# Performance work log

Measured on AMD Instinct MI355X. Metric: run time of the kernel, lower is better.

## Reference

```python
import jax, jax.numpy as jnp
import numpy as np

D_MODEL = 1024
N_HEADS = 16
D_HEAD = D_MODEL // N_HEADS
BLOCK = 128
B, T = 2, 2048


def setup_inputs() -> dict:
    key = jax.random.key(0)
    ks = jax.random.split(key, 5)
    x = jax.random.normal(ks[0], (B, T, D_MODEL), dtype=jnp.float32)
    def init_w(k):
        # nn.Linear default init scale ~ 1/sqrt(fan_in)
        return jax.random.normal(k, (D_MODEL, D_MODEL), dtype=jnp.float32) / np.sqrt(D_MODEL).astype(np.float32)
    return {
        "x": x,
        "Wq": init_w(ks[1]),
        "Wk": init_w(ks[2]),
        "Wv": init_w(ks[3]),
        "Wo": init_w(ks[4]),
    }


def _flash_attention(Q, K, V, block_size, scale):
    """Online-softmax tiled attention over kv blocks (causal). Q,K,V: (B,H,T,d)."""
    Bb, H, Tt, d = Q.shape
    n_blocks = Tt // block_size
    # (n_blocks, B, H, block, d) so scan streams kv tiles
    Kb = K.reshape(Bb, H, n_blocks, block_size, d).transpose(2, 0, 1, 3, 4)
    Vb = V.reshape(Bb, H, n_blocks, block_size, d).transpose(2, 0, 1, 3, 4)
    starts = jnp.arange(n_blocks) * block_size
    q_pos = jnp.arange(Tt)

    def step(carry, xs):
        m, l, acc = carry
        kb, vb, st = xs
        # scores: (B,H,T,block)
        scores = scale * jnp.einsum('bhtd,bhsd->bhts', Q, kb)
        kv_pos = st + jnp.arange(block_size)
        future = kv_pos[None, :] > q_pos[:, None]          # (T, block)
        scores = jnp.where(future[None, None], -jnp.inf, scores)
        m_new = jnp.maximum(m, jnp.max(scores, axis=-1, keepdims=True))
        p = jnp.exp(scores - m_new)
        corr = jnp.exp(m - m_new)
        l = corr * l + jnp.sum(p, axis=-1, keepdims=True)
        acc = corr * acc + jnp.einsum('bhts,bhsd->bhtd', p, vb)
        return (m_new, l, acc), None

    m0 = jnp.full((Bb, H, Tt, 1), -jnp.inf, dtype=jnp.float32)
    l0 = jnp.zeros((Bb, H, Tt, 1), dtype=jnp.float32)
    a0 = jnp.zeros((Bb, H, Tt, d), dtype=jnp.float32)
    (m, l, acc), _ = jax.lax.scan(step, (m0, l0, a0), (Kb, Vb, starts))
    return acc / jnp.maximum(l, 1e-12)


def reference(x, Wq, Wk, Wv, Wo):
    Bx, Tx, _ = x.shape
    scale = 1.0 / np.sqrt(D_HEAD).astype(np.float32)
    def proj(W):  # nn.Linear: y = x @ W.T
        y = jnp.einsum('btm,nm->btn', x, W)
        return y.reshape(Bx, Tx, N_HEADS, D_HEAD).transpose(0, 2, 1, 3)
    Q, K, V = proj(Wq), proj(Wk), proj(Wv)
    O = _flash_attention(Q.astype(jnp.float32), K.astype(jnp.float32), V.astype(jnp.float32), BLOCK, scale)
    O = O.astype(x.dtype).transpose(0, 2, 1, 3).reshape(Bx, Tx, D_MODEL)
    return jnp.einsum('btm,nm->btn', O, Wo)
```

## Files before the change

kernel.cpp:

```cpp
#include <hip/hip_runtime.h>
#include <hip/hip_bf16.h>

typedef __attribute__((ext_vector_type(8))) short short8;
typedef __attribute__((ext_vector_type(4))) float f32x4;
typedef __attribute__((ext_vector_type(16))) float f32x16;
typedef __attribute__((ext_vector_type(2))) unsigned int uint2v;
typedef __attribute__((ext_vector_type(4))) unsigned int uint4v;
typedef unsigned short u16;

#define MFMA_BF16(a, b, c) __builtin_amdgcn_mfma_f32_16x16x32_bf16(a, b, c, 0, 0, 0)
#define MFMA32(a, b, c) __builtin_amdgcn_mfma_f32_32x32x16_bf16(a, b, c, 0, 0, 0)

#define T_SEQ 2048
#define DMODEL 1024
#define NHEADS 16
#define DHEAD 64
#define NEG_BIG (-30000.0f)
#define QSCALE 0.1803368801111f
#define RESCALE_THR 8.0f

#if __has_builtin(__builtin_amdgcn_exp2f)
#define EXP2(x) __builtin_amdgcn_exp2f(x)
#else
#define EXP2(x) exp2f(x)
#endif

__device__ __forceinline__ unsigned bfr(unsigned u) {
  return (u + 0x7fffu + ((u >> 16) & 1u)) >> 16;
}
__device__ __forceinline__ uint4v ld8bf(const float* __restrict__ p) {
  const uint4v a = *(const uint4v*)p;
  const uint4v b = *(const uint4v*)(p + 4);
  uint4v r;
  r[0] = bfr(a[0]) | (bfr(a[1]) << 16);
  r[1] = bfr(a[2]) | (bfr(a[3]) << 16);
  r[2] = bfr(b[0]) | (bfr(b[1]) << 16);
  r[3] = bfr(b[2]) | (bfr(b[3]) << 16);
  return r;
}
__device__ __forceinline__ u16 f2bf(float f) {
  unsigned u = __float_as_uint(f);
  u += 0x7fffu + ((u >> 16) & 1u);
  return (u16)(u >> 16);
}
__device__ __forceinline__ unsigned pk2(float a, float b) {
  return (__float_as_uint(a) >> 16) | (__float_as_uint(b) & 0xffff0000u);
}
__device__ __forceinline__ void gld16(const u16* g, u16* l) {
  __builtin_amdgcn_global_load_lds(
      (const __attribute__((address_space(1))) unsigned int*)g,
      (__attribute__((address_space(3))) unsigned int*)l, 16, 0, 0);
}

__global__ __launch_bounds__(256) void cvt_all(
    const float* __restrict__ x, const float* __restrict__ wq,
    const float* __restrict__ wk, const float* __restrict__ wv,
    const float* __restrict__ wo, u16* __restrict__ xh, u16* __restrict__ wqh,
    u16* __restrict__ wkh, u16* __restrict__ wvh, u16* __restrict__ woh) {
  int bi = blockIdx.x;
  const float* s;
  u16* d;
  size_t base;
  if (bi < 2048) {
    s = x; d = xh; base = (size_t)bi * 2048;
  } else {
    int k = (bi - 2048) >> 9;
    int r = (bi - 2048) & 511;
    s = (k == 0) ? wq : (k == 1) ? wk : (k == 2) ? wv : wo;
    d = (k == 0) ? wqh : (k == 1) ? wkh : (k == 2) ? wvh : woh;
    base = (size_t)r * 2048;
  }
  size_t i = base + (size_t)threadIdx.x * 8;
  *(uint4v*)&d[i] = ld8bf(&s[i]);
}

__global__ __launch_bounds__(256) void gemm_qkv(
    const u16* __restrict__ X, const u16* __restrict__ Wq,
    const u16* __restrict__ Wk, const u16* __restrict__ Wv,
    u16* __restrict__ Qo, u16* __restrict__ Ko, u16* __restrict__ Vo) {
  __shared__ __attribute__((aligned(16))) u16 sm[16384];
  const int tid = threadIdx.x, lane = tid & 63, w = tid >> 6;
  const int wm = (w >> 1) * 64, wn = (w & 1) * 64;
  const int lrow = lane & 15;
  const int lk = (lane >> 4) << 3;
  const int lq = (lane >> 4) << 2;

  const int id = blockIdx.x;
  const int xcd = id & 7, r8 = id >> 3;
  const int xo = r8 & 3, yz = r8 >> 2;
  const int y = yz & 7, z = yz >> 3;
  const int mBase = (xcd * 4 + xo) * 128, nBase = y * 128;

  const u16* Bt = (z == 0) ? Wq : (z == 1) ? Wk : Wv;
  u16* D = (z == 0) ? Qo : (z == 1) ? Ko : Vo;
  const float scale = (z == 0) ? QSCALE : 1.0f;

  f32x4 acc[4][4];
#pragma unroll
  for (int mi = 0; mi < 4; mi++)
#pragma unroll
    for (int ni = 0; ni < 4; ni++) acc[mi][ni] = (f32x4)0.0f;

  auto stage = [&](int buf, int k0) {
#pragma unroll
    for (int i = 0; i < 2; i++) {
      int c = i * 256 + tid;
      int r = c >> 2, kk = (c & 3) << 3;
      gld16(&X[(size_t)(mBase + r) * 1024 + k0 + kk], &sm[buf * 4096 + c * 8]);
      gld16(&Bt[(size_t)(nBase + r) * 1024 + k0 + kk],
            &sm[8192 + buf * 4096 + c * 8]);
    }
  };

  stage(0, 0);
  __syncthreads();
  int cur = 0;
  for (int k0 = 0; k0 < 1024; k0 += 32) {
    if (k0 + 32 < 1024) stage(cur ^ 1, k0 + 32);
    short8 af[4], bf[4];
#pragma unroll
    for (int mi = 0; mi < 4; mi++)
      af[mi] = *(const short8*)&sm[cur * 4096 + (wm + mi * 16 + lrow) * 32 + lk];
#pragma unroll
    for (int ni = 0; ni < 4; ni++)
      bf[ni] =
          *(const short8*)&sm[8192 + cur * 4096 + (wn + ni * 16 + lrow) * 32 + lk];
#pragma unroll
    for (int mi = 0; mi < 4; mi++)
#pragma unroll
      for (int ni = 0; ni < 4; ni++)
        acc[mi][ni] = MFMA_BF16(af[mi], bf[ni], acc[mi][ni]);
    __syncthreads();
    cur ^= 1;
  }

  if (z != 2) {
#pragma unroll
    for (int mi = 0; mi < 4; mi++)
#pragma unroll
      for (int r = 0; r < 4; r++) {
        int m = mBase + wm + mi * 16 + lq + r;
        int b = m >> 11, t = m & 2047;
#pragma unroll
        for (int ni = 0; ni < 4; ni++) {
          int n = nBase + wn + ni * 16 + lrow;
          int h = n >> 6, dd = n & 63;
          D[(((size_t)(b * NHEADS + h)) * T_SEQ + t) * DHEAD + dd] =
              f2bf(acc[mi][ni][r] * scale);
        }
      }
  } else {
    u16* TT = &sm[w * 4096];
#pragma unroll
    for (int mi = 0; mi < 4; mi++)
#pragma unroll
      for (int r = 0; r < 4; r++) {
        int t_loc = mi * 16 + lq + r;
#pragma unroll
        for (int ni = 0; ni < 4; ni++) {
          int d_loc = ni * 16 + lrow;
          TT[d_loc * 64 + ((((t_loc >> 3) ^ (d_loc & 7)) << 3) | (t_loc & 7))] =
              f2bf(acc[mi][ni][r]);
        }
      }
    const int b = (mBase + wm) >> 11;
    const int t0 = (mBase + wm) & 2047;
#pragma unroll
    for (int it = 0; it < 8; it++) {
      int d_loc = it * 8 + (lane >> 3);
      int ch = lane & 7;
      short8 v = *(const short8*)&TT[d_loc * 64 + ((ch ^ (d_loc & 7)) << 3)];
      int n = nBase + wn + d_loc;
      int h = n >> 6, dd = n & 63;
      *(uint4v*)&D[(((size_t)((b * NHEADS + h) * DHEAD + dd)) * T_SEQ) + t0 +
                   ch * 8] = *(const uint4v*)&v;
    }
  }
}

__global__ __launch_bounds__(512, 4) void attn_qt32(
    const u16* __restrict__ Qg, const u16* __restrict__ Kg,
    const u16* __restrict__ Vtg, u16* __restrict__ Ob) {
  __shared__ __attribute__((aligned(16))) u16 smem[32768];

  const int tid = threadIdx.x;
  const int w = tid >> 6, lane = tid & 63;
  const int g = w >> 2;
  const int wg = w & 3;
  const int l31 = lane & 31, h = lane >> 5;
  const int rsw = l31 & 7;

  const int id = blockIdx.x;
  const int half = id >> 8;
  const int x = id & 255;
  const int xcd = x & 7;
  const int u = x >> 3;
  const int bh = xcd * 4 + (u & 3);
  const int qp = u >> 2;
  const int qt = half ? (15 - qp) : qp;
  const int b = bh >> 4, hh = bh & 15;
  const int qb = qt << 7;
  const u16* Qp = Qg + (size_t)bh * T_SEQ * DHEAD;
  const u16* Kp = Kg + (size_t)bh * T_SEQ * DHEAD;
  const u16* Vp = Vtg + (size_t)bh * DHEAD * T_SEQ;
  const int lastT = 2 * qt + 1;

  auto stage_tile = [&](int T) {
    if (T > lastT) return;
    const int slot = T & 3;
    const int r = tid >> 3;
    const int sw = ((tid & 7) ^ (r & 7)) << 3;
    gld16(&Kp[(size_t)(T * 64 + r) * DHEAD + sw], &smem[slot * 4096 + tid * 8]);
    gld16(&Vp[(size_t)r * T_SEQ + T * 64 + sw],
          &smem[16384 + slot * 4096 + tid * 8]);
  };

  stage_tile(0);
  stage_tile(1);

  const int qg = qb + wg * 32 + l31;
  short8 qf[4];
#pragma unroll
  for (int ks = 0; ks < 4; ks++)
    qf[ks] = *(const short8*)&Qp[(size_t)qg * DHEAD + ks * 16 + h * 8];

  float mst = NEG_BIG, lst = 0.f;
  f32x16 oa0 = (f32x16)0.f, oa1 = (f32x16)0.f;
  __syncthreads();

  for (int s = 0; s <= qt; s++) {
    stage_tile(2 * s + 2);
    stage_tile(2 * s + 3);
    const int T = 2 * s + g;
    const u16* Kc = &smem[(T & 3) * 4096];
    const u16* Vc = &smem[16384 + (T & 3) * 4096];

#pragma unroll
    for (int kvt2 = 0; kvt2 < 2; kvt2++) {
      f32x16 S = (f32x16)0.f;
      __builtin_amdgcn_s_setprio(1);
#pragma unroll
      for (int ks = 0; ks < 4; ks++) {
        short8 kf = *(const short8*)&Kc[(kvt2 * 32 + l31) * 64 +
                                        (((ks * 2 + h) ^ rsw) << 3)];
        S = MFMA32(kf, qf[ks], S);
      }
      __builtin_amdgcn_s_setprio(0);

      if (s == qt) {
        const int kvb2 = T * 64 + kvt2 * 32 + 4 * h;
#pragma unroll
        for (int r = 0; r < 16; r++) {
          int kv = kvb2 + (r & 3) + 8 * (r >> 2);
          if (kv > qg) S[r] = NEG_BIG;
        }
      }

      float mx = NEG_BIG;
#pragma unroll
      for (int r = 0; r < 16; r += 4)
        mx = fmaxf(mx, fmaxf(fmaxf(S[r], S[r + 1]), fmaxf(S[r + 2], S[r + 3])));
      mx = fmaxf(mx, __shfl_xor(mx, 32));
      if (!__all(mx <= mst + RESCALE_THR)) {
        float mn = fmaxf(mst, mx);
        float corr = EXP2(mst - mn);
        mst = mn;
        lst *= corr;
#pragma unroll
        for (int r = 0; r < 16; r++) {
          oa0[r] *= corr;
          oa1[r] *= corr;
        }
      }
      float ls = 0.f;
#pragma unroll
      for (int r = 0; r < 16; r++) {
        float pv = EXP2(S[r] - mst);
        S[r] = pv;
        ls += pv;
      }
      ls += __shfl_xor(ls, 32);
      lst += ls;

#pragma unroll
      for (int ks2 = 0; ks2 < 2; ks2++) {
        unsigned P0 = pk2(S[8 * ks2 + 0], S[8 * ks2 + 1]);
        unsigned P1 = pk2(S[8 * ks2 + 2], S[8 * ks2 + 3]);
        unsigned P2 = pk2(S[8 * ks2 + 4], S[8 * ks2 + 5]);
        unsigned P3 = pk2(S[8 * ks2 + 6], S[8 * ks2 + 7]);
        unsigned R0 = __shfl_xor(P0, 32), R1 = __shfl_xor(P1, 32);
        unsigned R2 = __shfl_xor(P2, 32), R3 = __shfl_xor(P3, 32);
        uint4v fu;
        fu[0] = h ? R2 : P0;
        fu[1] = h ? R3 : P1;
        fu[2] = h ? P2 : R0;
        fu[3] = h ? P3 : R1;
        short8 pf = *(short8*)&fu;
        const int kgr = kvt2 * 4 + ks2 * 2 + h;
        __builtin_amdgcn_s_setprio(1);
        short8 vf0 = *(const short8*)&Vc[l31 * 64 + ((kgr ^ rsw) << 3)];
        oa0 = MFMA32(vf0, pf, oa0);
        short8 vf1 = *(const short8*)&Vc[(32 + l31) * 64 + ((kgr ^ rsw) << 3)];
        oa1 = MFMA32(vf1, pf, oa1);
        __builtin_amdgcn_s_setprio(0);
      }
    }
    __syncthreads();
  }

  float* O1 = (float*)smem;
  float* ml = (float*)&smem[16384];
  const int q = wg * 32 + l31;
  if (g == 1) {
#pragma unroll
    for (int dt = 0; dt < 2; dt++)
#pragma unroll
      for (int t4 = 0; t4 < 4; t4++) {
        int gr = dt * 8 + t4 * 2 + h;
        int swg = (gr & 8) | ((gr & 7) ^ (q & 7));
        f32x4 v;
#pragma unroll
        for (int j = 0; j < 4; j++) v[j] = dt ? oa1[t4 * 4 + j] : oa0[t4 * 4 + j];
        *(f32x4*)&O1[q * 64 + swg * 4] = v;
      }
    if (h == 0) {
      ml[q] = mst;
      ml[128 + q] = lst;
    }
  }
  __syncthreads();
  if (g == 0) {
    const float m1 = ml[q], l1 = ml[128 + q];
    const float M = fmaxf(mst, m1);
    const float c0 = EXP2(mst - M), c1 = EXP2(m1 - M);
    const float inv = 1.f / (c0 * lst + c1 * l1);
    size_t rowbase = ((size_t)(b * T_SEQ + qb + q)) * DMODEL + hh * DHEAD;
#pragma unroll
    for (int dt = 0; dt < 2; dt++)
#pragma unroll
      for (int t4 = 0; t4 < 4; t4++) {
        int gr = dt * 8 + t4 * 2 + h;
        int swg = (gr & 8) | ((gr & 7) ^ (q & 7));
        f32x4 o1 = *(const f32x4*)&O1[q * 64 + swg * 4];
        float a0 = (c0 * (dt ? oa1[t4 * 4 + 0] : oa0[t4 * 4 + 0]) + c1 * o1[0]) * inv;
        float a1 = (c0 * (dt ? oa1[t4 * 4 + 1] : oa0[t4 * 4 + 1]) + c1 * o1[1]) * inv;
        float a2 = (c0 * (dt ? oa1[t4 * 4 + 2] : oa0[t4 * 4 + 2]) + c1 * o1[2]) * inv;
        float a3 = (c0 * (dt ? oa1[t4 * 4 + 3] : oa0[t4 * 4 + 3]) + c1 * o1[3]) * inv;
        uint2v pk;
        pk[0] = (unsigned)f2bf(a0) | ((unsigned)f2bf(a1) << 16);
        pk[1] = (unsigned)f2bf(a2) | ((unsigned)f2bf(a3) << 16);
        *(uint2v*)&Ob[rowbase + dt * 32 + t4 * 8 + 4 * h] = pk;
      }
  }
}

__global__ __launch_bounds__(256) void gemm_out_bf(const u16* __restrict__ O,
                                                   const u16* __restrict__ Wo,
                                                   float* __restrict__ Out) {
  __shared__ __attribute__((aligned(16))) u16 As[2][128 * 32];
  __shared__ __attribute__((aligned(16))) u16 Bs[2][64 * 32];
  const int tid = threadIdx.x, lane = tid & 63, w = tid >> 6;
  const int wm = (w >> 1) * 64, wn = (w & 1) * 32;
  const int lrow = lane & 15;
  const int lk = (lane >> 4) << 3;
  const int lq = (lane >> 4) << 2;

  const int id = blockIdx.x;
  const int xcd = id & 7, r8 = id >> 3;
  const int xo = r8 & 3, y = r8 >> 2;
  const int mBase = (xcd * 4 + xo) * 128, nBase = y * 64;

  f32x4 acc[4][2];
#pragma unroll
  for (int mi = 0; mi < 4; mi++)
#pragma unroll
    for (int ni = 0; ni < 2; ni++) acc[mi][ni] = (f32x4)0.0f;

  auto stage = [&](int buf, int k0) {
#pragma unroll
    for (int i = 0; i < 2; i++) {
      int c = i * 256 + tid;
      int r = c >> 2, kk = (c & 3) << 3;
      gld16(&O[(size_t)(mBase + r) * 1024 + k0 + kk], &As[buf][c * 8]);
    }
    int r = tid >> 2, kk = (tid & 3) << 3;
    gld16(&Wo[(size_t)(nBase + r) * 1024 + k0 + kk], &Bs[buf][tid * 8]);
  };

  stage(0, 0);
  __syncthreads();
  int cur = 0;
  for (int k0 = 0; k0 < 1024; k0 += 32) {
    if (k0 + 32 < 1024) stage(cur ^ 1, k0 + 32);
    short8 af[4], bf[2];
#pragma unroll
    for (int mi = 0; mi < 4; mi++)
      af[mi] = *(const short8*)&As[cur][(wm + mi * 16 + lrow) * 32 + lk];
#pragma unroll
    for (int ni = 0; ni < 2; ni++)
      bf[ni] = *(const short8*)&Bs[cur][(wn + ni * 16 + lrow) * 32 + lk];
#pragma unroll
    for (int mi = 0; mi < 4; mi++)
#pragma unroll
      for (int ni = 0; ni < 2; ni++)
        acc[mi][ni] = MFMA_BF16(af[mi], bf[ni], acc[mi][ni]);
    __syncthreads();
    cur ^= 1;
  }
#pragma unroll
  for (int mi = 0; mi < 4; mi++)
#pragma unroll
    for (int r = 0; r < 4; r++) {
      int m = mBase + wm + mi * 16 + lq + r;
#pragma unroll
      for (int ni = 0; ni < 2; ni++)
        Out[(size_t)m * DMODEL + nBase + wn + ni * 16 + lrow] = acc[mi][ni][r];
    }
}

extern "C" void kernel_launch(void* const* d_in, const int* in_sizes, int n_in,
                              void* d_out, int out_size, void* d_ws,
                              size_t ws_size, hipStream_t stream) {
  const float* x = (const float*)d_in[0];
  const float* Wq = (const float*)d_in[1];
  const float* Wk = (const float*)d_in[2];
  const float* Wv = (const float*)d_in[3];
  const float* Wo = (const float*)d_in[4];
  float* out = (float*)d_out;

  u16* xh = (u16*)d_ws;
  u16* wqh = xh + 4194304;
  u16* wkh = wqh + 1048576;
  u16* wvh = wkh + 1048576;
  u16* woh = wvh + 1048576;
  u16* Q = woh + 1048576;
  u16* K = Q + 4194304;
  u16* V = K + 4194304;
  u16* O = V + 4194304;

  cvt_all<<<dim3(4096), 256, 0, stream>>>(x, Wq, Wk, Wv, Wo, xh, wqh, wkh, wvh, woh);
  gemm_qkv<<<dim3(768), 256, 0, stream>>>(xh, wqh, wkh, wvh, Q, K, V);
  attn_qt32<<<dim3(512), 512, 0, stream>>>(Q, K, V, O);
  gemm_out_bf<<<dim3(512), 256, 0, stream>>>(O, woh, out);
}
```

Before: 171.1 us.

## Shrink attention query tile to 64 rows with 256-thread blocks and double buffer

The attention kernel now uses 64-query tiles in 256-thread blocks (4 waves, two kv-split groups) across 1024 blocks instead of 128-query tiles in 512-thread blocks. Shared memory is halved and the K/V staging becomes a simple two-slot scheme with syncs before and after each load. The change trades async prefetch overlap for more, smaller blocks, aiming at better occupancy and causal load balance. The risk is exposed global-load latency, since loads are no longer overlapped with compute, and more K/V reloads per head.

```diff
diff --git a/kernel.cpp b/kernel.cpp
--- a/kernel.cpp
+++ b/kernel.cpp
@@ -178,45 +178,45 @@
   }
 }
 
-__global__ __launch_bounds__(512, 4) void attn_qt32(
+__global__ __launch_bounds__(256, 4) void attn_q64(
     const u16* __restrict__ Qg, const u16* __restrict__ Kg,
     const u16* __restrict__ Vtg, u16* __restrict__ Ob) {
-  __shared__ __attribute__((aligned(16))) u16 smem[32768];
+  __shared__ __attribute__((aligned(16))) u16 smem[16384];
 
   const int tid = threadIdx.x;
   const int w = tid >> 6, lane = tid & 63;
-  const int g = w >> 2;
-  const int wg = w & 3;
+  const int g = w >> 1;
+  const int wg = w & 1;
   const int l31 = lane & 31, h = lane >> 5;
   const int rsw = l31 & 7;
 
   const int id = blockIdx.x;
-  const int half = id >> 8;
-  const int x = id & 255;
-  const int xcd = x & 7;
-  const int u = x >> 3;
-  const int bh = xcd * 4 + (u & 3);
-  const int qp = u >> 2;
-  const int qt = half ? (15 - qp) : qp;
+  const int seg = id >> 8;
+  const int xcd = id & 7;
+  const int bsub = (id >> 3) & 3;
+  const int qv = (id >> 5) & 7;
+  const int qt = (seg & 1) ? (seg * 8 + 7 - qv) : (seg * 8 + qv);
+  const int bh = xcd * 4 + bsub;
   const int b = bh >> 4, hh = bh & 15;
-  const int qb = qt << 7;
+  const int qb = qt << 6;
   const u16* Qp = Qg + (size_t)bh * T_SEQ * DHEAD;
   const u16* Kp = Kg + (size_t)bh * T_SEQ * DHEAD;
   const u16* Vp = Vtg + (size_t)bh * DHEAD * T_SEQ;
-  const int lastT = 2 * qt + 1;
 
   auto stage_tile = [&](int T) {
-    if (T > lastT) return;
-    const int slot = T & 3;
-    const int r = tid >> 3;
-    const int sw = ((tid & 7) ^ (r & 7)) << 3;
-    gld16(&Kp[(size_t)(T * 64 + r) * DHEAD + sw], &smem[slot * 4096 + tid * 8]);
-    gld16(&Vp[(size_t)r * T_SEQ + T * 64 + sw],
-          &smem[16384 + slot * 4096 + tid * 8]);
+    if (T > qt) return;
+    const int slot = T & 1;
+#pragma unroll
+    for (int i = 0; i < 2; i++) {
+      int c = i * 256 + tid;
+      int r = c >> 3;
+      int sw = ((c & 7) ^ (r & 7)) << 3;
+      gld16(&Kp[(size_t)(T * 64 + r) * DHEAD + sw],
+            &smem[slot * 4096 + c * 8]);
+      gld16(&Vp[(size_t)r * T_SEQ + T * 64 + sw],
+            &smem[8192 + slot * 4096 + c * 8]);
+    }
   };
-
-  stage_tile(0);
-  stage_tile(1);
 
   const int qg = qb + wg * 32 + l31;
   short8 qf[4];
@@ -226,90 +226,96 @@
 
   float mst = NEG_BIG, lst = 0.f;
   f32x16 oa0 = (f32x16)0.f, oa1 = (f32x16)0.f;
+
+  const int Smax = (qt + 2) >> 1;
+  for (int s = 0; s < Smax; s++) {
+    __syncthreads();
+    stage_tile(2 * s);
+    stage_tile(2 * s + 1);
+    __syncthreads();
+
+    const int T = 2 * s + g;
+    if (T <= qt) {
+      const u16* Kc = &smem[g * 4096];
+      const u16* Vc = &smem[8192 + g * 4096];
+
+#pragma unroll
+      for (int kvt2 = 0; kvt2 < 2; kvt2++) {
+        f32x16 S = (f32x16)0.f;
+        __builtin_amdgcn_s_setprio(1);
+#pragma unroll
+        for (int ks = 0; ks < 4; ks++) {
+          short8 kf = *(const short8*)&Kc[(kvt2 * 32 + l31) * 64 +
+                                          (((ks * 2 + h) ^ rsw) << 3)];
+          S = MFMA32(kf, qf[ks], S);
+        }
+        __builtin_amdgcn_s_setprio(0);
+
+        if (T == qt) {
+          const int kvb2 = T * 64 + kvt2 * 32 + 4 * h;
+#pragma unroll
+          for (int r = 0; r < 16; r++) {
+            int kv = kvb2 + (r & 3) + 8 * (r >> 2);
+            if (kv > qg) S[r] = NEG_BIG;
+          }
+        }
+
+        float mx = NEG_BIG;
+#pragma unroll
+        for (int r = 0; r < 16; r += 4)
+          mx = fmaxf(mx,
+                     fmaxf(fmaxf(S[r], S[r + 1]), fmaxf(S[r + 2], S[r + 3])));
+        mx = fmaxf(mx, __shfl_xor(mx, 32));
+        if (!__all(mx <= mst + RESCALE_THR)) {
+          float mn = fmaxf(mst, mx);
+          float corr = EXP2(mst - mn);
+          mst = mn;
+          lst *= corr;
+#pragma unroll
+          for (int r = 0; r < 16; r++) {
+            oa0[r] *= corr;
+            oa1[r] *= corr;
+          }
+        }
+        float ls = 0.f;
+#pragma unroll
+        for (int r = 0; r < 16; r++) {
+          float pv = EXP2(S[r] - mst);
+          S[r] = pv;
+          ls += pv;
+        }
+        ls += __shfl_xor(ls, 32);
+        lst += ls;
+
+#pragma unroll
+        for (int ks2 = 0; ks2 < 2; ks2++) {
+          unsigned P0 = pk2(S[8 * ks2 + 0], S[8 * ks2 + 1]);
+          unsigned P1 = pk2(S[8 * ks2 + 2], S[8 * ks2 + 3]);
+          unsigned P2 = pk2(S[8 * ks2 + 4], S[8 * ks2 + 5]);
+          unsigned P3 = pk2(S[8 * ks2 + 6], S[8 * ks2 + 7]);
+          unsigned R0 = __shfl_xor(P0, 32), R1 = __shfl_xor(P1, 32);
+          unsigned R2 = __shfl_xor(P2, 32), R3 = __shfl_xor(P3, 32);
+          uint4v fu;
+          fu[0] = h ? R2 : P0;
+          fu[1] = h ? R3 : P1;
+          fu[2] = h ? P2 : R0;
+          fu[3] = h ? P3 : R1;
+          short8 pf = *(short8*)&fu;
+          const int kgr = kvt2 * 4 + ks2 * 2 + h;
+          __builtin_amdgcn_s_setprio(1);
+          short8 vf0 = *(const short8*)&Vc[l31 * 64 + ((kgr ^ rsw) << 3)];
+          oa0 = MFMA32(vf0, pf, oa0);
+          short8 vf1 = *(const short8*)&Vc[(32 + l31) * 64 + ((kgr ^ rsw) << 3)];
+          oa1 = MFMA32(vf1, pf, oa1);
+          __builtin_amdgcn_s_setprio(0);
+        }
+      }
+    }
+  }
+
   __syncthreads();
-
-  for (int s = 0; s <= qt; s++) {
-    stage_tile(2 * s + 2);
-    stage_tile(2 * s + 3);
-    const int T = 2 * s + g;
-    const u16* Kc = &smem[(T & 3) * 4096];
-    const u16* Vc = &smem[16384 + (T & 3) * 4096];
-
-#pragma unroll
-    for (int kvt2 = 0; kvt2 < 2; kvt2++) {
-      f32x16 S = (f32x16)0.f;
-      __builtin_amdgcn_s_setprio(1);
-#pragma unroll
-      for (int ks = 0; ks < 4; ks++) {
-        short8 kf = *(const short8*)&Kc[(kvt2 * 32 + l31) * 64 +
-                                        (((ks * 2 + h) ^ rsw) << 3)];
-        S = MFMA32(kf, qf[ks], S);
-      }
-      __builtin_amdgcn_s_setprio(0);
-
-      if (s == qt) {
-        const int kvb2 = T * 64 + kvt2 * 32 + 4 * h;
-#pragma unroll
-        for (int r = 0; r < 16; r++) {
-          int kv = kvb2 + (r & 3) + 8 * (r >> 2);
-          if (kv > qg) S[r] = NEG_BIG;
-        }
-      }
-
-      float mx = NEG_BIG;
-#pragma unroll
-      for (int r = 0; r < 16; r += 4)
-        mx = fmaxf(mx, fmaxf(fmaxf(S[r], S[r + 1]), fmaxf(S[r + 2], S[r + 3])));
-      mx = fmaxf(mx, __shfl_xor(mx, 32));
-      if (!__all(mx <= mst + RESCALE_THR)) {
-        float mn = fmaxf(mst, mx);
-        float corr = EXP2(mst - mn);
-        mst = mn;
-        lst *= corr;
-#pragma unroll
-        for (int r = 0; r < 16; r++) {
-          oa0[r] *= corr;
-          oa1[r] *= corr;
-        }
-      }
-      float ls = 0.f;
-#pragma unroll
-      for (int r = 0; r < 16; r++) {
-        float pv = EXP2(S[r] - mst);
-        S[r] = pv;
-        ls += pv;
-      }
-      ls += __shfl_xor(ls, 32);
-      lst += ls;
-
-#pragma unroll
-      for (int ks2 = 0; ks2 < 2; ks2++) {
-        unsigned P0 = pk2(S[8 * ks2 + 0], S[8 * ks2 + 1]);
-        unsigned P1 = pk2(S[8 * ks2 + 2], S[8 * ks2 + 3]);
-        unsigned P2 = pk2(S[8 * ks2 + 4], S[8 * ks2 + 5]);
-        unsigned P3 = pk2(S[8 * ks2 + 6], S[8 * ks2 + 7]);
-        unsigned R0 = __shfl_xor(P0, 32), R1 = __shfl_xor(P1, 32);
-        unsigned R2 = __shfl_xor(P2, 32), R3 = __shfl_xor(P3, 32);
-        uint4v fu;
-        fu[0] = h ? R2 : P0;
-        fu[1] = h ? R3 : P1;
-        fu[2] = h ? P2 : R0;
-        fu[3] = h ? P3 : R1;
-        short8 pf = *(short8*)&fu;
-        const int kgr = kvt2 * 4 + ks2 * 2 + h;
-        __builtin_amdgcn_s_setprio(1);
-        short8 vf0 = *(const short8*)&Vc[l31 * 64 + ((kgr ^ rsw) << 3)];
-        oa0 = MFMA32(vf0, pf, oa0);
-        short8 vf1 = *(const short8*)&Vc[(32 + l31) * 64 + ((kgr ^ rsw) << 3)];
-        oa1 = MFMA32(vf1, pf, oa1);
-        __builtin_amdgcn_s_setprio(0);
-      }
-    }
-    __syncthreads();
-  }
-
   float* O1 = (float*)smem;
-  float* ml = (float*)&smem[16384];
+  float* ml = (float*)&smem[8192];
   const int q = wg * 32 + l31;
   if (g == 1) {
 #pragma unroll
@@ -325,12 +331,12 @@
       }
     if (h == 0) {
       ml[q] = mst;
-      ml[128 + q] = lst;
+      ml[64 + q] = lst;
     }
   }
   __syncthreads();
   if (g == 0) {
-    const float m1 = ml[q], l1 = ml[128 + q];
+    const float m1 = ml[q], l1 = ml[64 + q];
     const float M = fmaxf(mst, m1);
     const float c0 = EXP2(mst - M), c1 = EXP2(m1 - M);
     const float inv = 1.f / (c0 * lst + c1 * l1);
@@ -440,6 +446,6 @@
 
   cvt_all<<<dim3(4096), 256, 0, stream>>>(x, Wq, Wk, Wv, Wo, xh, wqh, wkh, wvh, woh);
   gemm_qkv<<<dim3(768), 256, 0, stream>>>(xh, wqh, wkh, wvh, Q, K, V);
-  attn_qt32<<<dim3(512), 512, 0, stream>>>(Q, K, V, O);
+  attn_q64<<<dim3(1024), 256, 0, stream>>>(Q, K, V, O);
   gemm_out_bf<<<dim3(512), 256, 0, stream>>>(O, woh, out);
 }
```

After: 177.4 us. 1.04x slower.
